# Kernel tuning notes

Hardware: AMD Instinct MI355X
Metric: run time of the kernel (lower is better)

The kernel has to match this reference:

```python
import jax, jax.numpy as jnp
from jax import lax
import numpy as np

B, D, H, T = 64, 32, 512, 1024


def setup_inputs() -> dict:
    key = jax.random.key(0)
    ks = jax.random.split(key, 7)
    s = 1.0 / np.sqrt(H)
    return {
        "input_data": jax.random.normal(ks[0], (B, D, T), dtype=jnp.float32),
        "W_ih": jax.random.uniform(ks[1], (4 * H, D), jnp.float32, -s, s),
        "W_hh": jax.random.uniform(ks[2], (4 * H, H), jnp.float32, -s, s),
        "b_ih": jax.random.uniform(ks[3], (4 * H,), jnp.float32, -s, s),
        "b_hh": jax.random.uniform(ks[4], (4 * H,), jnp.float32, -s, s),
        "conv_w": jax.random.uniform(ks[5], (1, H, 1), jnp.float32, -s, s),
        "conv_b": jax.random.uniform(ks[6], (1,), jnp.float32, -s, s),
    }


def reference(input_data, W_ih, W_hh, b_ih, b_hh, conv_w, conv_b):
    # (B, D, T) -> (T, B, D), seq-first like torch nn.LSTM
    x = jnp.transpose(input_data, (2, 0, 1))
    # Precompute input-to-gate projections for all timesteps: (T, B, 4H)
    xproj = jnp.einsum('tbd,gd->tbg', x, W_ih) + b_ih + b_hh
    h0 = jnp.zeros((x.shape[1], H), x.dtype)
    c0 = jnp.zeros((x.shape[1], H), x.dtype)

    def step(carry, xp):
        h, c = carry
        gates = xp + h @ W_hh.T  # (B, 4H)
        i, f, g, o = jnp.split(gates, 4, axis=-1)  # torch gate order: i, f, g, o
        i = jax.nn.sigmoid(i)
        f = jax.nn.sigmoid(f)
        g = jnp.tanh(g)
        o = jax.nn.sigmoid(o)
        c_new = f * c + i * g
        h_new = o * jnp.tanh(c_new)
        return (h_new, c_new), h_new

    _, hs = lax.scan(step, (h0, c0), xproj)  # hs: (T, B, H)
    out = jnp.transpose(hs, (1, 2, 0))  # (B, H, T)
    # Conv1d(H, 1, kernel=1) == per-timestep linear
    pred = jnp.einsum('bht,oh->bot', out, conv_w[:, :, 0]) + conv_b[:, None]
    return pred  # (B, 1, T)
```

## Files before the change

kernel.cpp:

```cpp
#include <hip/hip_runtime.h>
#include <hip/hip_bf16.h>


typedef unsigned short ushort_t;
typedef unsigned int   uint_t;
typedef unsigned long long u64_t;
typedef __attribute__((ext_vector_type(8))) short bf16x8;
typedef __attribute__((ext_vector_type(4))) float f32x4;
typedef __attribute__((ext_vector_type(4))) uint_t u32x4;

#define T_STEPS 1024
#define HID     512
#define KDIM    544
#define NBLK    64
#define NTHR    512

__device__ inline ushort_t f2bf(float x) {
    __hip_bfloat16 h = __float2bfloat16(x);
    return *(ushort_t*)&h;
}
__device__ inline float bf2f(ushort_t u) {
    __hip_bfloat16 h = *(__hip_bfloat16*)&u;
    return __bfloat162float(h);
}

__device__ inline f32x4 MFMA(bf16x8 a, bf16x8 b, f32x4 c) {
    return __builtin_amdgcn_mfma_f32_16x16x32_bf16(a, b, c, 0, 0, 0);
}

__device__ inline u32x4 cld16(const void* p) {
    u32x4 v;
    asm volatile("global_load_dwordx4 %0, %1, off sc0 sc1"
                 : "=v"(v) : "v"(p) : "memory");
    return v;
}
__device__ inline void cst4(void* p, uint_t v) {
    asm volatile("global_store_dword %0, %1, off sc0 sc1"
                 :: "v"(p), "v"(v) : "memory");
}
__device__ inline void waitvm0() {
    asm volatile("s_waitcnt vmcnt(0)" ::: "memory");
}

__device__ inline float act_gate(float v, int is_tanh) {
    float vc = fminf(fmaxf(v, -43.f), 43.f);
    float kk = is_tanh ? -2.88539008f : -1.44269504f;
    float e  = __builtin_exp2f(vc * kk);
    float num = is_tanh ? (1.f - e) : 1.f;
    return num * __builtin_amdgcn_rcpf(1.f + e);
}


__global__ void k_init(uint_t* hx32) {
    int i = blockIdx.x * 256 + threadIdx.x;
    hx32[i] = 0x00010000u;
}

__global__ void k_wcat(const float* __restrict__ wih, const float* __restrict__ whh,
                       ushort_t* __restrict__ wh, ushort_t* __restrict__ wl) {
    int r = blockIdx.x;
    for (int k = threadIdx.x; k < KDIM; k += 256) {
        float w = (k < 512) ? whh[r * 512 + k] : wih[r * 32 + (k - 512)];
        ushort_t hh = f2bf(w);
        ushort_t ll = f2bf(w - bf2f(hh));
        wh[r * KDIM + k] = hh;
        wl[r * KDIM + k] = ll;
    }
}

__global__ void k_xbuf(const float* __restrict__ in,
                       ushort_t* __restrict__ xh, ushort_t* __restrict__ xl) {
    __shared__ float tile[64][65];
    int bp = blockIdx.x >> 4;
    int tt = blockIdx.x & 15;
    int t0 = tt * 64;
    int wv = threadIdx.x >> 6, l = threadIdx.x & 63;
    for (int r = wv * 16; r < wv * 16 + 16; r++) {
        int b = bp * 2 + (r >> 5), d = r & 31;
        tile[r][l] = in[(b * 32 + d) * 1024 + t0 + l];
    }
    __syncthreads();
    for (int i = 0; i < 16; i++) {
        int tl = wv * 16 + i;
        float v = tile[l][tl];
        ushort_t hh = f2bf(v);
        ushort_t ll = f2bf(v - bf2f(hh));
        int o = (t0 + tl) * 2048 + bp * 64 + l;
        xh[o] = hh;
        xl[o] = ll;
    }
}

__global__ void k_reduce(const float* __restrict__ part, float* __restrict__ out,
                         const float* __restrict__ cvb) {
    int b = blockIdx.x >> 2;
    int t = (blockIdx.x & 3) * 256 + threadIdx.x;
    int g = b >> 4, bl = b & 15;
    const float* p = part + ((size_t)(g * 16 * 16 + bl)) * 1024 + t;
    float sum = 0.f;
    #pragma unroll
    for (int s = 0; s < 16; s++) sum += p[(size_t)s * 16 * 1024];
    out[b * 1024 + t] = sum + cvb[0];
}


__global__ __launch_bounds__(NTHR, 2) void k_lstm(
    const ushort_t* __restrict__ wh, const ushort_t* __restrict__ wlo,
    const ushort_t* __restrict__ xh, const ushort_t* __restrict__ xl,
    char* hx,
    const float* __restrict__ bih, const float* __restrict__ bhh,
    const float* __restrict__ convw, float* __restrict__ part)
{
    const int tid = threadIdx.x;
    const int w   = tid >> 6;
    const int l   = tid & 63;
    const int g   = blockIdx.x >> 4;
    const int s   = blockIdx.x & 15;
    const int n   = l & 15;
    const int q   = l >> 4;
    const int j   = s * 32 + w * 4 + q;
    const int roww = (n & 3) * HID + s * 32 + w * 4 + (n >> 2);
    const int b0  = g * 16;
    const int wg  = s * 8 + w;

    __shared__ u64_t hs[2][4096];
    __shared__ float projsh[8][16][32];

    bf16x8 Bh[17], Bl[17];
    #pragma unroll
    for (int c = 0; c < 17; c++) {
        Bh[c] = *(const bf16x8*)(wh  + roww * KDIM + c * 32 + q * 8);
        Bl[c] = *(const bf16x8*)(wlo + roww * KDIM + c * 32 + q * 8);
    }

    float bias4[4];
    #pragma unroll
    for (int r = 0; r < 4; r++) bias4[r] = bih[r * HID + j] + bhh[r * HID + j];
    const float cw = convw[j];
    float cst = 0.f;

    const int m16 = tid & 15;
    const int hi5 = tid >> 4;
    const int sq  = (hi5 >> 1) & 3, sd = hi5 & 1, sc0v = hi5 >> 3;

    __syncthreads();

    union frag { u64_t d[2]; bf16x8 v; };

    for (int t = 0; t < T_STEPS; t++) {
        frag Ax, Lx;
        {
            int xo = (t * 64 + b0 + n) * 32 + q * 8;
            Ax.v = *(const bf16x8*)(xh + xo);
            Lx.v = *(const bf16x8*)(xl + xo);
        }

        const char* srcB = hx + (size_t)(((t & 1) * 4 + g)) * 32768 + tid * 16;
        u32x4 hv[4];
        #pragma unroll
        for (int k = 0; k < 4; k++) hv[k] = cld16(srcB + k * 8192);
        waitvm0();
        if (t > 0) {
            const uint_t exp = ((uint_t)(((t - 1) >> 1) & 1)) << 16;
            for (;;) {
                bool ok = true;
                #pragma unroll
                for (int k = 0; k < 4; k++) {
                    if (((hv[k][0] & 0x10000u) != exp) ||
                        ((hv[k][1] & 0x10000u) != exp) ||
                        ((hv[k][2] & 0x10000u) != exp) ||
                        ((hv[k][3] & 0x10000u) != exp)) {
                        hv[k] = cld16(srcB + k * 8192);
                        ok = false;
                    }
                }
                if (ok) break;
                __builtin_amdgcn_s_sleep(1);
                waitvm0();
            }
        }
        {
            const int buf = t & 1;
            #pragma unroll
            for (int k = 0; k < 4; k++) {
                uint_t I0 = hv[k][0], I1 = hv[k][1];
                uint_t I2 = hv[k][2], I3 = hv[k][3];
                uint_t hA = __builtin_amdgcn_perm(I1, I0, 0x05040100u);
                uint_t hB = __builtin_amdgcn_perm(I3, I2, 0x05040100u);
                uint_t lA = __builtin_amdgcn_perm(I1, I0, 0x07060302u);
                uint_t lB = __builtin_amdgcn_perm(I3, I2, 0x07060302u);
                int c  = k * 4 + sc0v;
                int li = ((c * 4 + sq) * 16 + m16) * 2 + sd;
                hs[buf][li]        = (u64_t)hA | ((u64_t)hB << 32);
                hs[buf][li + 2048] = (u64_t)lA | ((u64_t)lB << 32);
            }
        }
        __syncthreads();

        const int buf = t & 1;
        f32x4 a0 = {0,0,0,0}, a1 = {0,0,0,0}, a2 = {0,0,0,0},
              a3 = {0,0,0,0}, a4 = {0,0,0,0}, a5 = {0,0,0,0};
        #pragma unroll
        for (int c = 0; c < 16; c++) {
            frag Ah, Al;
            int li = ((c * 4 + q) * 16 + n) * 2;
            Ah.v = *(const bf16x8*)&hs[buf][li];
            Al.v = *(const bf16x8*)&hs[buf][li + 2048];
            if (c & 1) {
                a1 = MFMA(Bh[c], Ah.v, a1);
                a3 = MFMA(Bl[c], Ah.v, a3);
                a5 = MFMA(Bh[c], Al.v, a5);
            } else {
                a0 = MFMA(Bh[c], Ah.v, a0);
                a2 = MFMA(Bl[c], Ah.v, a2);
                a4 = MFMA(Bh[c], Al.v, a4);
            }
        }
        {
            a0 = MFMA(Bh[16], Ax.v, a0);
            a2 = MFMA(Bl[16], Ax.v, a2);
            a4 = MFMA(Bh[16], Lx.v, a4);
        }
        f32x4 D = (a0 + a1) + (a2 + a3) + (a4 + a5);

        char* dstB = hx + (size_t)((((t + 1) & 1) * 4 + g) * 128 + wg) * 256;
        const uint_t tag32 = ((uint_t)((t >> 1) & 1)) << 16;
        float iv = act_gate(D[0] + bias4[0], 0);
        float fv = act_gate(D[1] + bias4[1], 0);
        float gv = act_gate(D[2] + bias4[2], 1);
        float ov = act_gate(D[3] + bias4[3], 0);
        float cc = fv * cst + iv * gv;
        cst = cc;
        float th = act_gate(cc, 1);
        float h  = ov * th;
        float pr = cw * h;
        {
            ushort_t hb = f2bf(h);
            uint_t hvp = (uint_t)hb;
            uint_t lvp = (uint_t)f2bf(h - bf2f(hb));
            uint_t word = (hvp | (lvp << 16)) & ~0x10000u;
            word |= tag32;
            cst4(dstB + n * 16 + q * 4, word);
        }

        pr += __shfl_xor(pr, 16);
        pr += __shfl_xor(pr, 32);
        if (l < 16) projsh[w][l][t & 31] = pr;
        if ((t & 31) == 31) {
            __syncthreads();
            int b = tid >> 5, tl = tid & 31;
            float v = ((projsh[0][b][tl] + projsh[1][b][tl]) +
                       (projsh[2][b][tl] + projsh[3][b][tl])) +
                      ((projsh[4][b][tl] + projsh[5][b][tl]) +
                       (projsh[6][b][tl] + projsh[7][b][tl]));
            float* dpt = part + (size_t)((g * 16 + s) * 16 + b) * 1024 + (t - 31);
            __builtin_nontemporal_store(v, dpt + tl);
            __syncthreads();
        }
    }
}

extern "C" void kernel_launch(void* const* d_in, const int* in_sizes, int n_in,
                              void* d_out, int out_size, void* d_ws, size_t ws_size,
                              hipStream_t stream) {
    const float* in  = (const float*)d_in[0];
    const float* Wih = (const float*)d_in[1];
    const float* Whh = (const float*)d_in[2];
    const float* bih = (const float*)d_in[3];
    const float* bhh = (const float*)d_in[4];
    const float* cvw = (const float*)d_in[5];
    const float* cvb = (const float*)d_in[6];
    float* out = (float*)d_out;

    char* ws = (char*)d_ws;
    ushort_t* wh  = (ushort_t*)ws; ws += (size_t)2048 * KDIM * 2;
    ushort_t* wl  = (ushort_t*)ws; ws += (size_t)2048 * KDIM * 2;
    ushort_t* xh  = (ushort_t*)ws; ws += (size_t)1024 * 64 * 32 * 2;
    ushort_t* xl  = (ushort_t*)ws; ws += (size_t)1024 * 64 * 32 * 2;
    char*     hx  = ws;            ws += (size_t)2 * 4 * 128 * 16 * 16;
    float*    pp  = (float*)ws;    ws += (size_t)64 * 16 * 1024 * 4;

    k_init<<<256, 256, 0, stream>>>((uint_t*)hx);
    k_wcat<<<2048, 256, 0, stream>>>(Wih, Whh, wh, wl);
    k_xbuf<<<512, 256, 0, stream>>>(in, xh, xl);
    k_lstm<<<NBLK, NTHR, 0, stream>>>(wh, wl, xh, xl, hx,
                                      bih, bhh, cvw, pp);
    k_reduce<<<256, 256, 0, stream>>>(pp, out, cvb);
}
```

Before: 3.061 ms.

## Split hidden-state polling into two halves overlapped with recurrent MFMAs

Each step's exchange of the hidden state between blocks is split into two halves. The first half (chunks 0-7) is polled and staged to LDS. The loads for the second half are issued before the first-half MFMAs run, so waiting on other blocks overlaps with compute. The LDS staging buffer goes from double to single buffering, which is safe because the two halves touch disjoint regions. The cost is an extra __syncthreads per timestep and macro-unrolled weight registers.

```diff
diff --git a/kernel.cpp b/kernel.cpp
--- a/kernel.cpp
+++ b/kernel.cpp
@@ -104,6 +104,64 @@
 }
 
 
+#define POLL2(kA, kB) do {                                              \
+    const uint_t exp_ = ((uint_t)(((t - 1) >> 1) & 1)) << 16;           \
+    for (;;) {                                                          \
+        bool ok_ = true;                                                \
+        if (((hv[kA][0] & 0x10000u) != exp_) ||                         \
+            ((hv[kA][1] & 0x10000u) != exp_) ||                         \
+            ((hv[kA][2] & 0x10000u) != exp_) ||                         \
+            ((hv[kA][3] & 0x10000u) != exp_)) {                         \
+            hv[kA] = cld16(srcB + (kA) * 8192);                         \
+            ok_ = false;                                                \
+        }                                                               \
+        if (((hv[kB][0] & 0x10000u) != exp_) ||                         \
+            ((hv[kB][1] & 0x10000u) != exp_) ||                         \
+            ((hv[kB][2] & 0x10000u) != exp_) ||                         \
+            ((hv[kB][3] & 0x10000u) != exp_)) {                         \
+            hv[kB] = cld16(srcB + (kB) * 8192);                         \
+            ok_ = false;                                                \
+        }                                                               \
+        if (ok_) break;                                                 \
+        __builtin_amdgcn_s_sleep(1);                                    \
+        waitvm0();                                                      \
+        __builtin_amdgcn_sched_barrier(0);                              \
+    }                                                                   \
+} while (0)
+
+#define STAGE1(k_) do {                                                 \
+    uint_t I0 = hv[k_][0], I1 = hv[k_][1];                              \
+    uint_t I2 = hv[k_][2], I3 = hv[k_][3];                              \
+    uint_t hA_ = __builtin_amdgcn_perm(I1, I0, 0x05040100u);            \
+    uint_t hB_ = __builtin_amdgcn_perm(I3, I2, 0x05040100u);            \
+    uint_t lA_ = __builtin_amdgcn_perm(I1, I0, 0x07060302u);            \
+    uint_t lB_ = __builtin_amdgcn_perm(I3, I2, 0x07060302u);            \
+    int c_  = (k_) * 4 + sc0v;                                          \
+    int li_ = ((c_ * 4 + sq) * 16 + m16) * 2 + sd;                      \
+    hs[li_]        = (u64_t)hA_ | ((u64_t)hB_ << 32);                   \
+    hs[li_ + 2048] = (u64_t)lA_ | ((u64_t)lB_ << 32);                   \
+} while (0)
+
+#define CHUNK(c) do {                                                   \
+    frag Ah_, Al_;                                                      \
+    int li_ = (((c) * 4 + q) * 16 + n) * 2;                             \
+    Ah_.v = *(const bf16x8*)&hs[li_];                                   \
+    Al_.v = *(const bf16x8*)&hs[li_ + 2048];                            \
+    if ((c) & 1) {                                                      \
+        a1 = MFMA(Bh##c, Ah_.v, a1);                                    \
+        a3 = MFMA(Bl##c, Ah_.v, a3);                                    \
+        a5 = MFMA(Bh##c, Al_.v, a5);                                    \
+    } else {                                                            \
+        a0 = MFMA(Bh##c, Ah_.v, a0);                                    \
+        a2 = MFMA(Bl##c, Ah_.v, a2);                                    \
+        a4 = MFMA(Bh##c, Al_.v, a4);                                    \
+    }                                                                   \
+} while (0)
+
+#define DECLW(c)                                                        \
+    const bf16x8 Bh##c = *(const bf16x8*)(wbh + (c) * 32);              \
+    const bf16x8 Bl##c = *(const bf16x8*)(wbl + (c) * 32);
+
 __global__ __launch_bounds__(NTHR, 2) void k_lstm(
     const ushort_t* __restrict__ wh, const ushort_t* __restrict__ wlo,
     const ushort_t* __restrict__ xh, const ushort_t* __restrict__ xl,
@@ -123,15 +181,14 @@
     const int b0  = g * 16;
     const int wg  = s * 8 + w;
 
-    __shared__ u64_t hs[2][4096];
+    __shared__ u64_t hs[4096];
     __shared__ float projsh[8][16][32];
 
-    bf16x8 Bh[17], Bl[17];
-    #pragma unroll
-    for (int c = 0; c < 17; c++) {
-        Bh[c] = *(const bf16x8*)(wh  + roww * KDIM + c * 32 + q * 8);
-        Bl[c] = *(const bf16x8*)(wlo + roww * KDIM + c * 32 + q * 8);
-    }
+    const ushort_t* wbh = wh  + roww * KDIM + q * 8;
+    const ushort_t* wbl = wlo + roww * KDIM + q * 8;
+    DECLW(0)  DECLW(1)  DECLW(2)  DECLW(3)  DECLW(4)  DECLW(5)
+    DECLW(6)  DECLW(7)  DECLW(8)  DECLW(9)  DECLW(10) DECLW(11)
+    DECLW(12) DECLW(13) DECLW(14) DECLW(15) DECLW(16)
 
     float bias4[4];
     #pragma unroll
@@ -148,78 +205,45 @@
     union frag { u64_t d[2]; bf16x8 v; };
 
     for (int t = 0; t < T_STEPS; t++) {
-        frag Ax, Lx;
+        bf16x8 Ax, Lx;
         {
             int xo = (t * 64 + b0 + n) * 32 + q * 8;
-            Ax.v = *(const bf16x8*)(xh + xo);
-            Lx.v = *(const bf16x8*)(xl + xo);
+            Ax = *(const bf16x8*)(xh + xo);
+            Lx = *(const bf16x8*)(xl + xo);
         }
 
         const char* srcB = hx + (size_t)(((t & 1) * 4 + g)) * 32768 + tid * 16;
         u32x4 hv[4];
-        #pragma unroll
-        for (int k = 0; k < 4; k++) hv[k] = cld16(srcB + k * 8192);
+        hv[0] = cld16(srcB);
+        hv[1] = cld16(srcB + 8192);
         waitvm0();
-        if (t > 0) {
-            const uint_t exp = ((uint_t)(((t - 1) >> 1) & 1)) << 16;
-            for (;;) {
-                bool ok = true;
-                #pragma unroll
-                for (int k = 0; k < 4; k++) {
-                    if (((hv[k][0] & 0x10000u) != exp) ||
-                        ((hv[k][1] & 0x10000u) != exp) ||
-                        ((hv[k][2] & 0x10000u) != exp) ||
-                        ((hv[k][3] & 0x10000u) != exp)) {
-                        hv[k] = cld16(srcB + k * 8192);
-                        ok = false;
-                    }
-                }
-                if (ok) break;
-                __builtin_amdgcn_s_sleep(1);
-                waitvm0();
-            }
-        }
-        {
-            const int buf = t & 1;
-            #pragma unroll
-            for (int k = 0; k < 4; k++) {
-                uint_t I0 = hv[k][0], I1 = hv[k][1];
-                uint_t I2 = hv[k][2], I3 = hv[k][3];
-                uint_t hA = __builtin_amdgcn_perm(I1, I0, 0x05040100u);
-                uint_t hB = __builtin_amdgcn_perm(I3, I2, 0x05040100u);
-                uint_t lA = __builtin_amdgcn_perm(I1, I0, 0x07060302u);
-                uint_t lB = __builtin_amdgcn_perm(I3, I2, 0x07060302u);
-                int c  = k * 4 + sc0v;
-                int li = ((c * 4 + sq) * 16 + m16) * 2 + sd;
-                hs[buf][li]        = (u64_t)hA | ((u64_t)hB << 32);
-                hs[buf][li + 2048] = (u64_t)lA | ((u64_t)lB << 32);
-            }
-        }
+        __builtin_amdgcn_sched_barrier(0);
+        if (t > 0) POLL2(0, 1);
+        STAGE1(0);
+        STAGE1(1);
         __syncthreads();
 
-        const int buf = t & 1;
+        hv[2] = cld16(srcB + 16384);
+        hv[3] = cld16(srcB + 24576);
+
         f32x4 a0 = {0,0,0,0}, a1 = {0,0,0,0}, a2 = {0,0,0,0},
               a3 = {0,0,0,0}, a4 = {0,0,0,0}, a5 = {0,0,0,0};
-        #pragma unroll
-        for (int c = 0; c < 16; c++) {
-            frag Ah, Al;
-            int li = ((c * 4 + q) * 16 + n) * 2;
-            Ah.v = *(const bf16x8*)&hs[buf][li];
-            Al.v = *(const bf16x8*)&hs[buf][li + 2048];
-            if (c & 1) {
-                a1 = MFMA(Bh[c], Ah.v, a1);
-                a3 = MFMA(Bl[c], Ah.v, a3);
-                a5 = MFMA(Bh[c], Al.v, a5);
-            } else {
-                a0 = MFMA(Bh[c], Ah.v, a0);
-                a2 = MFMA(Bl[c], Ah.v, a2);
-                a4 = MFMA(Bh[c], Al.v, a4);
-            }
-        }
+        CHUNK(0); CHUNK(1); CHUNK(2); CHUNK(3);
+        CHUNK(4); CHUNK(5); CHUNK(6); CHUNK(7);
+
+        waitvm0();
+        __builtin_amdgcn_sched_barrier(0);
+        if (t > 0) POLL2(2, 3);
+        STAGE1(2);
+        STAGE1(3);
+        __syncthreads();
+
+        CHUNK(8);  CHUNK(9);  CHUNK(10); CHUNK(11);
+        CHUNK(12); CHUNK(13); CHUNK(14); CHUNK(15);
         {
-            a0 = MFMA(Bh[16], Ax.v, a0);
-            a2 = MFMA(Bl[16], Ax.v, a2);
-            a4 = MFMA(Bh[16], Lx.v, a4);
+            a0 = MFMA(Bh16, Ax, a0);
+            a2 = MFMA(Bl16, Ax, a2);
+            a4 = MFMA(Bh16, Lx, a4);
         }
         f32x4 D = (a0 + a1) + (a2 + a3) + (a4 + a5);
 
```

Result: faster. 2.991 ms (-2.3%).
